# Performance work log

Measured on AMD Instinct MI355X. Metric: run time of the kernel, lower is better.

## Reference

```python
import jax, jax.numpy as jnp
import numpy as np

VECT = 300   # word-vector dim
H = 128      # GRU hidden size
NSTACK = 3   # MultiHead stacks (shared SelfAttention weights)
SEQ = 4096


def _ln(x, g, b, eps=1e-5):
    m = jnp.mean(x, axis=-1, keepdims=True)
    v = jnp.mean((x - m) ** 2, axis=-1, keepdims=True)
    return g * (x - m) / jnp.sqrt(v + eps) + b


def _multihead(x, q_w, q_b, k_w, k_b, v_w, v_b, aln_g, aln_b, w_w, w_b, mln_g, mln_b):
    # x: [S, 300]. Same attention weights reused for all 3 stacks (as in source).
    scale = jnp.sqrt(jnp.asarray(float(VECT), x.dtype))
    out = x
    for _ in range(NSTACK):
        q = out @ q_w.T + q_b
        k = out @ k_w.T + k_b
        v = out @ v_w.T + v_b
        a = jax.nn.softmax((q @ k.T) / scale, axis=1)      # [S, S]
        h = _ln(a @ v + out, aln_g, aln_b)                  # SelfAttention out
        out = _ln(h @ w_w.T + w_b + x, mln_g, mln_b)        # residual to original x
    return out


def _gru(xs, w_ih, w_hh, b_ih, b_hh):
    # xs: [S, VECT]; PyTorch GRUCell math, h0 = zeros. Input projections batched.
    gx = xs @ w_ih.T + b_ih  # [S, 3H]
    def step(h, g):
        gh = h @ w_hh.T + b_hh
        r = jax.nn.sigmoid(g[:H] + gh[:H])
        z = jax.nn.sigmoid(g[H:2 * H] + gh[H:2 * H])
        n = jnp.tanh(g[2 * H:] + r * gh[2 * H:])
        return (1.0 - z) * n + z * h, None
    h, _ = jax.lax.scan(step, jnp.zeros((H,), xs.dtype), gx)
    return h


def setup_inputs() -> dict:
    key = jax.random.key(0)
    ks = jax.random.split(key, 16)

    def lin(k, o, i, s=0.05):
        k1, k2 = jax.random.split(k)
        return (jax.random.normal(k1, (o, i), jnp.float32) * s,
                jax.random.normal(k2, (o,), jnp.float32) * s)

    q_w, q_b = lin(ks[0], VECT, VECT)
    k_w, k_b = lin(ks[1], VECT, VECT)
    v_w, v_b = lin(ks[2], VECT, VECT)
    w_w, w_b = lin(ks[3], VECT, VECT)
    g1_wih, g1_bih = lin(ks[4], 3 * H, VECT)
    g1_whh, g1_bhh = lin(ks[5], 3 * H, H)
    g2_wih, g2_bih = lin(ks[6], 3 * H, VECT)
    g2_whh, g2_bhh = lin(ks[7], 3 * H, H)
    fc1_w, fc1_b = lin(ks[8], 256, 2 * H)
    fc2_w, fc2_b = lin(ks[9], 3, 256)

    return {
        'x1': jax.random.normal(ks[10], (SEQ, VECT), jnp.float32),
        'x2': jax.random.normal(ks[11], (SEQ, VECT), jnp.float32),
        'q_w': q_w, 'q_b': q_b, 'k_w': k_w, 'k_b': k_b, 'v_w': v_w, 'v_b': v_b,
        'aln_g': jnp.ones((VECT,), jnp.float32), 'aln_b': jnp.zeros((VECT,), jnp.float32),
        'w_w': w_w, 'w_b': w_b,
        'mln_g': jnp.ones((VECT,), jnp.float32), 'mln_b': jnp.zeros((VECT,), jnp.float32),
        'g1_wih': g1_wih, 'g1_whh': g1_whh, 'g1_bih': g1_bih, 'g1_bhh': g1_bhh,
        'g2_wih': g2_wih, 'g2_whh': g2_whh, 'g2_bih': g2_bih, 'g2_bhh': g2_bhh,
        'fc1_w': fc1_w, 'fc1_b': fc1_b, 'fc2_w': fc2_w, 'fc2_b': fc2_b,
    }


def reference(x1, x2, q_w, q_b, k_w, k_b, v_w, v_b, aln_g, aln_b, w_w, w_b,
              mln_g, mln_b, g1_wih, g1_whh, g1_bih, g1_bhh,
              g2_wih, g2_whh, g2_bih, g2_bhh, fc1_w, fc1_b, fc2_w, fc2_b):
    a1 = _multihead(x1, q_w, q_b, k_w, k_b, v_w, v_b, aln_g, aln_b, w_w, w_b, mln_g, mln_b)
    a2 = _multihead(x2, q_w, q_b, k_w, k_b, v_w, v_b, aln_g, aln_b, w_w, w_b, mln_g, mln_b)
    h1 = _gru(a1, g1_wih, g1_whh, g1_bih, g1_bhh)  # [H]
    h2 = _gru(a2, g2_wih, g2_whh, g2_bih, g2_bhh)  # [H]
    h = jnp.concatenate([h1, h2])[None, :]          # [1, 2H]
    h = jax.nn.relu(h @ fc1_w.T + fc1_b)
    return jax.nn.log_softmax(h @ fc2_w.T + fc2_b, axis=1)  # [1, 3]
```

## Files before the change

### kernel.cpp

```cpp
#include <hip/hip_runtime.h>
#include <hip/hip_bf16.h>

#define SEQL 4096
#define VECT 300
#define DP   320
#define NQT  20
#define HN   128
#define G3   384
#define JC   4
#define KROW 328
#define VROW 40
#define PROW 40

typedef unsigned short u16;
typedef unsigned char  u8;
typedef __attribute__((ext_vector_type(8))) short bf16x8;
typedef __attribute__((ext_vector_type(4))) float f32x4;
typedef __attribute__((ext_vector_type(4))) unsigned int u32x4;
typedef __attribute__((ext_vector_type(8))) int   v8i;

#define MFMA(a,b,c) __builtin_amdgcn_mfma_f32_16x16x32_bf16(a,b,c,0,0,0)

#define L2E 1.44269504088896f

#define RAW_BAR() do {                                          \
    asm volatile("s_waitcnt lgkmcnt(0)" ::: "memory");          \
    __builtin_amdgcn_s_barrier();                               \
    asm volatile("" ::: "memory");                              \
} while (0)

__device__ __forceinline__ float bf2f(u16 v){
    union { unsigned u; float f; } t; t.u = ((unsigned)v) << 16; return t.f;
}
__device__ __forceinline__ u16 f2bf(float f){
    union { float f; unsigned u; } t; t.f = f;
    return (u16)((t.u + 0x7FFFu + ((t.u >> 16) & 1u)) >> 16);
}
__device__ __forceinline__ float sigm_f(float x){
    return __builtin_amdgcn_rcpf(1.f + __builtin_amdgcn_exp2f(-L2E * x));
}
__device__ __forceinline__ float tanh_f(float x){
    return fmaf(2.f, __builtin_amdgcn_rcpf(1.f + __builtin_amdgcn_exp2f(-2.f * L2E * x)), -1.f);
}
__device__ __forceinline__ float sel4(f32x4 v, int r){
    float a = (r & 1) ? v.y : v.x;
    float b = (r & 1) ? v.w : v.z;
    return (r & 2) ? b : a;
}

__global__ __launch_bounds__(256) void pad_x2(const float* __restrict__ x1, const float* __restrict__ x2,
                                              float* __restrict__ xf, u16* __restrict__ cur)
{
    int s = blockIdx.y;
    const float* src = s ? x2 : x1;
    float* xfo = xf + (long)s * SEQL * DP;
    u16*  cro = cur + (long)s * SEQL * DP;
    int n = SEQL * DP;
    for (int i = blockIdx.x * blockDim.x + threadIdx.x; i < n; i += gridDim.x * blockDim.x){
        int r = i / DP, c = i - r * DP;
        float v = (c < VECT) ? src[r * VECT + c] : 0.f;
        xfo[i] = v;
        cro[i] = f2bf(v);
    }
}

__global__ __launch_bounds__(256) void cvt_pad_w4(const float* __restrict__ w0, const float* __restrict__ w1,
                                                  const float* __restrict__ w2, const float* __restrict__ w3,
                                                  u16* __restrict__ Wpk)
{
    int sl = blockIdx.y;
    const float* src = (sl == 0) ? w0 : (sl == 1) ? w1 : (sl == 2) ? w2 : w3;
    u16* dst = Wpk + (long)sl * DP * DP;
    int n = DP * DP;
    for (int i = blockIdx.x * blockDim.x + threadIdx.x; i < n; i += gridDim.x * blockDim.x){
        int r = i / DP, c = i - r * DP;
        float v = (r < VECT && c < VECT) ? src[r * VECT + c] : 0.f;
        dst[i] = f2bf(v);
    }
}

__global__ __launch_bounds__(256) void cvt_pad_g2(const float* __restrict__ w0, const float* __restrict__ w1,
                                                  u16* __restrict__ GWpk)
{
    int s = blockIdx.y;
    const float* src = s ? w1 : w0;
    u16* dst = GWpk + (long)s * G3 * DP;
    int n = G3 * DP;
    for (int i = blockIdx.x * blockDim.x + threadIdx.x; i < n; i += gridDim.x * blockDim.x){
        int r = i / DP, c = i - r * DP;
        float v = (c < VECT) ? src[r * VECT + c] : 0.f;
        dst[i] = f2bf(v);
    }
}

__global__ __launch_bounds__(256) void cvt_whh2(const float* __restrict__ w0, const float* __restrict__ w1,
                                                u8* __restrict__ dst0)
{
    int s = blockIdx.y;
    const float* src = s ? w1 : w0;
    u8* dst = dst0 + (long)s * G3 * HN;
    int idx = blockIdx.x * 256 + threadIdx.x;
    if (idx >= G3 * HN) return;
    int prow = idx >> 7, col = idx & 127;
    int w  = prow / 48, rem = prow - w * 48;
    int g  = rem >> 4;  int rr = rem & 15;
    int orow = g * 128 + w * 16 + rr;
    int pk = __builtin_amdgcn_cvt_pk_fp8_f32(src[orow * HN + col], 0.f, 0, false);
    dst[idx] = (u8)(pk & 0xFF);
}

template<int NT, int OM, bool WPERSEQ>
__global__ __launch_bounds__(256) void gemm_k(
    const u16* __restrict__ A, const u16* __restrict__ Wp,
    const float* __restrict__ b0, const float* __restrict__ b1, const float* __restrict__ b2,
    int nb, void* __restrict__ Out)
{
    const int lane = threadIdx.x & 63;
    const int wid  = threadIdx.x >> 6;
    const int s    = blockIdx.z;
    const int sl   = blockIdx.y;
    const int wsel = WPERSEQ ? s : sl;
    const int row0 = blockIdx.x * 64 + wid * 16;
    const int m    = lane & 15;
    const int q    = lane >> 4;

    const u16* Arow = A + ((long)s * SEQL + row0) * DP;
    const u16* W    = Wp + (long)wsel * (NT * 16) * DP;

    f32x4 zf = {0.f, 0.f, 0.f, 0.f};
    f32x4 acc[NT];
    #pragma unroll
    for (int n = 0; n < NT; n++) acc[n] = zf;

    for (int c = 0; c < DP / 32; ++c){
        const int koff = c * 32 + q * 8;
        bf16x8 a0 = *(const bf16x8*)(Arow + m * DP + koff);
        #pragma unroll
        for (int n = 0; n < NT; n++){
            bf16x8 b = *(const bf16x8*)(W + (n * 16 + m) * DP + koff);
            acc[n] = MFMA(a0, b, acc[n]);
        }
    }

    const int bsel = WPERSEQ ? s : sl;
    const float* bp = (bsel == 0) ? b0 : ((bsel == 1) ? b1 : b2);
    const long SLC = 2L * SEQL * DP;

    #pragma unroll
    for (int n = 0; n < NT; n++){
        int col = n * 16 + m;
        float bv = (col < nb) ? bp[col] : 0.f;
        #pragma unroll
        for (int r = 0; r < 4; r++){
            long row = row0 + q * 4 + r;
            float v = acc[n][r] + bv;
            if (OM == 4){
                int g = col >> 7, i2 = col & 127;
                long off = ((long)s * SEQL + row) * (long)(NT * 16) + (i2 * 3 + g);
                ((float*)Out)[off] = v;
            } else {
                long off;
                if (sl < 2) off = ((long)(sl * 2 + s) * SEQL + row) * DP + col;
                else        off = 2 * SLC + ((long)s * DP + col) * SEQL + row;
                ((u16*)Out)[off] = f2bf(v);
            }
        }
    }
}

__global__ __launch_bounds__(256) void gemmln_k(
    const u16* __restrict__ A, const u16* __restrict__ Wp, const float* __restrict__ bias,
    const float* __restrict__ res0, const float* __restrict__ res1,
    const float* __restrict__ g, const float* __restrict__ b,
    u16* __restrict__ OutB, float* __restrict__ OutF)
{
    const int lane = threadIdx.x & 63;
    const int wid  = threadIdx.x >> 6;
    const int s    = blockIdx.z;
    const int row0 = blockIdx.x * 64 + wid * 16;
    const int m    = lane & 15;
    const int q    = lane >> 4;

    const u16* Arow = A + ((long)s * SEQL + row0) * DP;
    const float* res = s ? res1 : res0;

    f32x4 zf = {0.f, 0.f, 0.f, 0.f};
    f32x4 acc[NQT];
    #pragma unroll
    for (int n = 0; n < NQT; n++) acc[n] = zf;

    for (int c = 0; c < DP / 32; ++c){
        const int koff = c * 32 + q * 8;
        bf16x8 a0 = *(const bf16x8*)(Arow + m * DP + koff);
        #pragma unroll
        for (int n = 0; n < NQT; n++){
            bf16x8 bb = *(const bf16x8*)(Wp + (n * 16 + m) * DP + koff);
            acc[n] = MFMA(a0, bb, acc[n]);
        }
    }

    float sum[4] = {0,0,0,0}, sq[4] = {0,0,0,0};
    #pragma unroll
    for (int n = 0; n < NQT; n++){
        int col = n * 16 + m;
        float bv = (col < VECT) ? bias[col] : 0.f;
        #pragma unroll
        for (int r = 0; r < 4; r++){
            long row = row0 + q * 4 + r;
            float rr = (col < VECT) ? res[row * VECT + col] : 0.f;
            float t = (col < VECT) ? (acc[n][r] + bv + rr) : 0.f;
            acc[n][r] = t;
            sum[r] += t; sq[r] += t * t;
        }
    }
    #pragma unroll
    for (int r = 0; r < 4; r++){
        float su = sum[r], sv = sq[r];
        su += __shfl_xor(su, 1); sv += __shfl_xor(sv, 1);
        su += __shfl_xor(su, 2); sv += __shfl_xor(sv, 2);
        su += __shfl_xor(su, 4); sv += __shfl_xor(sv, 4);
        su += __shfl_xor(su, 8); sv += __shfl_xor(sv, 8);
        sum[r] = su; sq[r] = sv;
    }
    float mean[4], rstd[4];
    #pragma unroll
    for (int r = 0; r < 4; r++){
        mean[r] = sum[r] / VECT;
        float var = sq[r] / VECT - mean[r] * mean[r];
        rstd[r] = rsqrtf(var + 1e-5f);
    }
    #pragma unroll
    for (int n = 0; n < NQT; n++){
        int col = n * 16 + m;
        float gv = (col < VECT) ? g[col] : 0.f;
        float bv = (col < VECT) ? b[col] : 0.f;
        #pragma unroll
        for (int r = 0; r < 4; r++){
            long row = (long)s * SEQL + row0 + q * 4 + r;
            float t = (col < VECT) ? ((acc[n][r] - mean[r]) * rstd[r] * gv + bv) : 0.f;
            OutB[row * DP + col] = f2bf(t);
            OutF[row * DP + col] = t;
        }
    }
}

__global__ __launch_bounds__(256, 2) void flash_k(
    const u16* __restrict__ Q, const u16* __restrict__ K, const u16* __restrict__ VT,
    u16* __restrict__ Onum, float* __restrict__ Lp)
{
    const int tid  = threadIdx.x;
    const int lane = tid & 63;
    const int wid  = tid >> 6;
    const int bid  = blockIdx.x;
    const int s    = bid & 1;
    const int jc   = (bid >> 1) & 3;
    const int xi   = bid >> 3;
    const int row0 = xi * 64 + wid * 16;
    const int m = lane & 15, q = lane >> 4;

    __shared__ __align__(16) u16 Kt[32 * KROW];
    __shared__ __align__(16) u16 Vt[DP * VROW];
    __shared__ __align__(16) u16 pb[4][16 * PROW];

    const u16* Qb = Q  + ((long)s * SEQL + row0) * DP;
    const u16* Kc = K  + (long)s * SEQL * DP + (long)jc * 1024 * DP;
    const u16* Vc = VT + (long)s * DP * SEQL + jc * 1024;

    bf16x8 qf[10];
    #pragma unroll
    for (int c = 0; c < 10; c++)
        qf[c] = *(const bf16x8*)(Qb + m * DP + c * 32 + q * 8);

    int skoff[5], wkoff[5], svoff[5], wvoff[5];
    #pragma unroll
    for (int it = 0; it < 5; it++){
        int f  = (it * 256 + tid) * 8;
        int rk = f / 320, ck = f - rk * 320;
        skoff[it] = f;
        wkoff[it] = rk * KROW + ck;
        int rv = f >> 5, cv = f & 31;
        svoff[it] = rv * SEQL + cv;
        wvoff[it] = rv * VROW + cv;
    }

    f32x4 zf = {0.f, 0.f, 0.f, 0.f};
    f32x4 oacc[NQT];
    #pragma unroll
    for (int n = 0; n < NQT; n++) oacc[n] = zf;
    float lacc[4] = {0,0,0,0};

    const float K2 = 0.057735026918962576f * L2E;
    const float MB = -16.f * L2E;

    u32x4 kreg[5], vreg[5];
    #pragma unroll
    for (int it = 0; it < 5; it++){
        kreg[it] = *(const u32x4*)(Kc + skoff[it]);
        vreg[it] = *(const u32x4*)(Vc + svoff[it]);
    }
    #pragma unroll
    for (int it = 0; it < 5; it++){
        *(u32x4*)(&Kt[wkoff[it]]) = kreg[it];
        *(u32x4*)(&Vt[wvoff[it]]) = vreg[it];
    }
    RAW_BAR();

    u16* pbw = &pb[wid][0];

    for (int j = 0; j < 32; ++j){
        if (j + 1 < 32){
            const u16* Kj = Kc + (j + 1) * 32 * DP;
            const u16* Vj = Vc + (j + 1) * 32;
            #pragma unroll
            for (int it = 0; it < 5; it++){
                kreg[it] = *(const u32x4*)(Kj + skoff[it]);
                vreg[it] = *(const u32x4*)(Vj + svoff[it]);
            }
        }
        f32x4 sA = zf, sB = zf;
        #pragma unroll
        for (int c = 0; c < 10; c++){
            bf16x8 kA = *(const bf16x8*)(&Kt[(m     ) * KROW + c * 32 + q * 8]);
            bf16x8 kB = *(const bf16x8*)(&Kt[(m + 16) * KROW + c * 32 + q * 8]);
            sA = MFMA(qf[c], kA, sA);
            sB = MFMA(qf[c], kB, sB);
        }
        #pragma unroll
        for (int r = 0; r < 4; r++){
            float a = __builtin_amdgcn_exp2f(fmaf(sA[r], K2, MB));
            float b = __builtin_amdgcn_exp2f(fmaf(sB[r], K2, MB));
            lacc[r] += a + b;
            pbw[(q * 4 + r) * PROW +      m] = f2bf(a);
            pbw[(q * 4 + r) * PROW + 16 + m] = f2bf(b);
        }
        bf16x8 pf = *(const bf16x8*)(&pbw[m * PROW + q * 8]);
        #pragma unroll
        for (int n = 0; n < NQT; n++){
            bf16x8 vb = *(const bf16x8*)(&Vt[(n * 16 + m) * VROW + q * 8]);
            oacc[n] = MFMA(pf, vb, oacc[n]);
        }
        RAW_BAR();
        if (j + 1 < 32){
            #pragma unroll
            for (int it = 0; it < 5; it++){
                *(u32x4*)(&Kt[wkoff[it]]) = kreg[it];
                *(u32x4*)(&Vt[wvoff[it]]) = vreg[it];
            }
        }
        RAW_BAR();
    }

    #pragma unroll
    for (int r = 0; r < 4; r++){
        float t0 = lacc[r];
        t0 += __shfl_xor(t0, 1); t0 += __shfl_xor(t0, 2);
        t0 += __shfl_xor(t0, 4); t0 += __shfl_xor(t0, 8);
        lacc[r] = t0;
    }
    const long grow0 = (long)s * SEQL + row0;
    if (m == 0){
        #pragma unroll
        for (int r = 0; r < 4; r++)
            Lp[(long)jc * 2 * SEQL + grow0 + q * 4 + r] = lacc[r];
    }
    u16* Ob = Onum + ((long)jc * 2 * SEQL + grow0) * DP;
    #pragma unroll
    for (int n = 0; n < NQT; n++)
        #pragma unroll
        for (int r = 0; r < 4; r++)
            Ob[(long)(q * 4 + r) * DP + n * 16 + m] = f2bf(oacc[n][r]);
}

__global__ __launch_bounds__(256) void lncomb_k(const u16* __restrict__ Onum, const float* __restrict__ Lp,
                                                const float* __restrict__ XF,
                                                const float* __restrict__ g, const float* __restrict__ b,
                                                u16* __restrict__ OutB)
{
    long row = (long)((blockIdx.x * blockDim.x + threadIdx.x) >> 6);
    int lane = threadIdx.x & 63;
    if (row >= 2L * SEQL) return;
    float l = 0.f;
    #pragma unroll
    for (int jc = 0; jc < JC; jc++) l += Lp[(long)jc * 2 * SEQL + row];
    float inv = 1.f / l;
    const float* xr = XF + row * DP;
    float v[5], sum = 0.f, sq = 0.f;
    #pragma unroll
    for (int i = 0; i < 5; i++){
        int c = lane + i * 64;
        float o = 0.f;
        #pragma unroll
        for (int jc = 0; jc < JC; jc++)
            o += bf2f(Onum[((long)jc * 2 * SEQL + row) * DP + c]);
        float t = (c < VECT) ? (o * inv + xr[c]) : 0.f;
        v[i] = t; sum += t; sq += t * t;
    }
    #pragma unroll
    for (int o = 1; o < 64; o <<= 1){ sum += __shfl_xor(sum, o); sq += __shfl_xor(sq, o); }
    float mean = sum / VECT;
    float var  = sq / VECT - mean * mean;
    float rstd = rsqrtf(var + 1e-5f);
    #pragma unroll
    for (int i = 0; i < 5; i++){
        int c = lane + i * 64;
        float t = (c < VECT) ? ((v[i] - mean) * rstd * g[c] + b[c]) : 0.f;
        OutB[row * DP + c] = f2bf(t);
    }
}

__global__ __launch_bounds__(512, 1) void gru_k(
    const float* __restrict__ GXP,
    const u8* __restrict__ Whh8p,
    const float* __restrict__ Bhh1, const float* __restrict__ Bhh2,
    float* __restrict__ Hout)
{
    const int s = blockIdx.x;
    const int tid = threadIdx.x;
    const int lane = tid & 63;
    const int wid  = tid >> 6;
    const int m = lane & 15, q = lane >> 4;
    const u8* Whh = Whh8p + (long)s * G3 * HN;
    const float* Bhh = s ? Bhh2 : Bhh1;
    const float* gx = GXP + (long)s * SEQL * G3;

    __shared__ __align__(8) u8 hst[2][HN];

    v8i af[3];
    #pragma unroll
    for (int g = 0; g < 3; g++)
        af[g] = *(const v8i*)(Whh + (long)(wid * 48 + g * 16 + m) * HN + q * 32);

    const int rsel = m & 3;
    const int il   = wid * 16 + q * 4 + rsel;
    const int il3  = il * 3;
    const float bhr = Bhh[il], bhz = Bhh[HN + il], bhn = Bhh[2 * HN + il];

    if (tid < HN){ hst[0][tid] = 0; hst[1][tid] = 0; }

    const float* ga = gx + il3;
    float cr0 = ga[0], cz0 = ga[1], cn0 = ga[2];
    const float* gb = gx + G3 + il3;
    float cr1 = gb[0], cz1 = gb[1], cn1 = gb[2];

    __syncthreads();

    float h = 0.f;
    const f32x4 zf = {0.f, 0.f, 0.f, 0.f};

#define GRU_STEP(T, CR, CZ, CN, WB, RB)                                               \
    {                                                                                 \
        v8i bfrag = *(const v8i*)(&hst[RB][q * 32]);                                  \
        f32x4 a0 = __builtin_amdgcn_mfma_scale_f32_16x16x128_f8f6f4(af[0], bfrag, zf, 0, 0, 0, 127, 0, 127); \
        f32x4 a1 = __builtin_amdgcn_mfma_scale_f32_16x16x128_f8f6f4(af[1], bfrag, zf, 0, 0, 0, 127, 0, 127); \
        f32x4 a2 = __builtin_amdgcn_mfma_scale_f32_16x16x128_f8f6f4(af[2], bfrag, zf, 0, 0, 0, 127, 0, 127); \
        float ghr = sel4(a0, rsel);                                                   \
        float ghz = sel4(a1, rsel);                                                   \
        float ghn = sel4(a2, rsel);                                                   \
        float rg = sigm_f(CR + ghr + bhr);                                            \
        float zg = sigm_f(CZ + ghz + bhz);                                            \
        float ng = tanh_f(CN + rg * (ghn + bhn));                                     \
        h = (1.f - zg) * ng + zg * h;                                                 \
        if (m < 4){                                                                   \
            int pk = __builtin_amdgcn_cvt_pk_fp8_f32(h, h, 0, false);                 \
            hst[WB][il] = (u8)(pk & 0xFF);                                            \
        }                                                                             \
        int tp = ((T) + 2 < SEQL) ? (T) + 2 : SEQL - 1;                               \
        const float* gp = gx + (long)tp * G3 + il3;                                   \
        CR = gp[0]; CZ = gp[1]; CN = gp[2];                                           \
        asm volatile("s_waitcnt lgkmcnt(0)" ::: "memory");                            \
        __builtin_amdgcn_s_barrier();                                                 \
        asm volatile("" ::: "memory");                                                \
    }

    for (int t = 0; t < SEQL; t += 2){
        GRU_STEP(t,     cr0, cz0, cn0, 0, 1);
        GRU_STEP(t + 1, cr1, cz1, cn1, 1, 0);
    }
#undef GRU_STEP

    if (m < 4) Hout[s * HN + il] = h;
}

__global__ __launch_bounds__(256) void final_k(const float* __restrict__ Hout,
                                               const float* __restrict__ fc1w, const float* __restrict__ fc1b,
                                               const float* __restrict__ fc2w, const float* __restrict__ fc2b,
                                               float* __restrict__ out)
{
    __shared__ float hb[256];
    __shared__ float r1[256];
    __shared__ float lg[3];
    int tid = threadIdx.x;
    hb[tid] = Hout[tid];
    __syncthreads();
    float a = 0.f;
    for (int k2 = 0; k2 < 256; k2++) a += hb[k2] * fc1w[tid * 256 + k2];
    a += fc1b[tid];
    r1[tid] = fmaxf(a, 0.f);
    __syncthreads();
    if (tid < 3){
        float v = 0.f;
        for (int k2 = 0; k2 < 256; k2++) v += r1[k2] * fc2w[tid * 256 + k2];
        lg[tid] = v + fc2b[tid];
    }
    __syncthreads();
    if (tid == 0){
        float mx = fmaxf(lg[0], fmaxf(lg[1], lg[2]));
        float se = __expf(lg[0] - mx) + __expf(lg[1] - mx) + __expf(lg[2] - mx);
        float ls = mx + logf(se);
        out[0] = lg[0] - ls;
        out[1] = lg[1] - ls;
        out[2] = lg[2] - ls;
    }
}

extern "C" void kernel_launch(void* const* d_in, const int* in_sizes, int n_in,
                              void* d_out, int out_size, void* d_ws, size_t ws_size,
                              hipStream_t stream)
{
    (void)in_sizes; (void)n_in; (void)out_size; (void)ws_size;
    const float* x1     = (const float*)d_in[0];
    const float* x2     = (const float*)d_in[1];
    const float* q_w    = (const float*)d_in[2],  *q_b   = (const float*)d_in[3];
    const float* k_w    = (const float*)d_in[4],  *k_b   = (const float*)d_in[5];
    const float* v_w    = (const float*)d_in[6],  *v_b   = (const float*)d_in[7];
    const float* aln_g  = (const float*)d_in[8],  *aln_b = (const float*)d_in[9];
    const float* w_w    = (const float*)d_in[10], *w_b   = (const float*)d_in[11];
    const float* mln_g  = (const float*)d_in[12], *mln_b = (const float*)d_in[13];
    const float* g1_wih = (const float*)d_in[14], *g1_whh = (const float*)d_in[15];
    const float* g1_bih = (const float*)d_in[16], *g1_bhh = (const float*)d_in[17];
    const float* g2_wih = (const float*)d_in[18], *g2_whh = (const float*)d_in[19];
    const float* g2_bih = (const float*)d_in[20], *g2_bhh = (const float*)d_in[21];
    const float* fc1w   = (const float*)d_in[22], *fc1b  = (const float*)d_in[23];
    const float* fc2w   = (const float*)d_in[24], *fc2b  = (const float*)d_in[25];

    char* wsp = (char*)d_ws;
    auto alloc = [&](size_t bytes) -> char* {
        char* p = wsp; wsp += (bytes + 255) & ~(size_t)255; return p;
    };
    float* XF   = (float*)alloc(2L * SEQL * DP * 4);
    u16*   CUR  = (u16*)  alloc(2L * SEQL * DP * 2);
    u16*   Hb   = (u16*)  alloc(2L * SEQL * DP * 2);
    u16*   Wpk  = (u16*)  alloc(4L * DP * DP * 2);
    u16*   GWpk = (u16*)  alloc(2L * G3 * DP * 2);
    u8*    Whh8 = (u8*)   alloc(2L * G3 * HN);
    float* Hout = (float*)alloc(2L * HN * 4);
    float* Lp   = (float*)alloc((long)JC * 2 * SEQL * 4);
    size_t u1 = (2L * 2 * SEQL * DP + 2L * DP * SEQL) * 2;
    size_t u1b = 2L * SEQL * G3 * 4;
    u16*   QKV  = (u16*)  alloc(u1 > u1b ? u1 : u1b);
    u16*   VT   = QKV + 2L * 2 * SEQL * DP;
    float* GX   = (float*)QKV;
    u16*   Onum = (u16*)  alloc((long)JC * 2 * SEQL * DP * 2);

    pad_x2<<<dim3(256, 2), 256, 0, stream>>>(x1, x2, XF, CUR);
    cvt_pad_w4<<<dim3(128, 4), 256, 0, stream>>>(q_w, k_w, v_w, w_w, Wpk);
    cvt_pad_g2<<<dim3(128, 2), 256, 0, stream>>>(g1_wih, g2_wih, GWpk);
    cvt_whh2<<<dim3(192, 2), 256, 0, stream>>>(g1_whh, g2_whh, Whh8);

    for (int st = 0; st < 3; ++st){
        gemm_k<NQT, 3, false><<<dim3(SEQL / 64, 3, 2), 256, 0, stream>>>(
            CUR, Wpk, q_b, k_b, v_b, VECT, QKV);
        flash_k<<<dim3(512), 256, 0, stream>>>(QKV, QKV + 2L*SEQL*DP, VT, Onum, Lp);
        lncomb_k<<<dim3(2 * SEQL / 4), 256, 0, stream>>>(Onum, Lp, XF, aln_g, aln_b, Hb);
        gemmln_k<<<dim3(SEQL / 64, 1, 2), 256, 0, stream>>>(
            Hb, Wpk + 3L * DP * DP, w_b, x1, x2, mln_g, mln_b, CUR, XF);
    }

    gemm_k<24, 4, true><<<dim3(SEQL / 64, 1, 2), 256, 0, stream>>>(
        CUR, GWpk, g1_bih, g2_bih, nullptr, G3, GX);
    gru_k<<<dim3(2), 512, 0, stream>>>(GX, Whh8, g1_bhh, g2_bhh, Hout);
    final_k<<<dim3(1), 256, 0, stream>>>(Hout, fc1w, fc1b, fc2w, fc2b, (float*)d_out);
}
```

Measured before the change: 2.008 ms.

## Fuse attention LayerNorm combine into output-projection GEMM via folded weights

Removes the separate lncomb kernel and the Hb intermediate buffer. The split-KV partial sums are combined per row inside the GEMM kernel, staged in LDS as bf16, and the first LayerNorm is applied after the matmul algebraically. The LN gamma is folded into the weight matrix, and the mean correction and beta contribution come from precomputed row sums. This saves one launch and a global write and read of the normalized activations per stack, at the cost of GEMM on un-normalized bf16 values (precision risk) and a small extra prep kernel.

After: 2.036 ms. No clear change (+1.4%).

```diff
diff --git a/kernel.cpp b/kernel.cpp
--- a/kernel.cpp
+++ b/kernel.cpp
@@ -11,6 +11,7 @@
 #define KROW 328
 #define VROW 40
 #define PROW 40
+#define AROW 328
 
 typedef unsigned short u16;
 typedef unsigned char  u8;
@@ -64,18 +65,44 @@
     }
 }
 
-__global__ __launch_bounds__(256) void cvt_pad_w4(const float* __restrict__ w0, const float* __restrict__ w1,
-                                                  const float* __restrict__ w2, const float* __restrict__ w3,
+__global__ __launch_bounds__(256) void cvt_pad_w3(const float* __restrict__ w0, const float* __restrict__ w1,
+                                                  const float* __restrict__ w2,
                                                   u16* __restrict__ Wpk)
 {
     int sl = blockIdx.y;
-    const float* src = (sl == 0) ? w0 : (sl == 1) ? w1 : (sl == 2) ? w2 : w3;
+    const float* src = (sl == 0) ? w0 : (sl == 1) ? w1 : w2;
     u16* dst = Wpk + (long)sl * DP * DP;
     int n = DP * DP;
     for (int i = blockIdx.x * blockDim.x + threadIdx.x; i < n; i += gridDim.x * blockDim.x){
         int r = i / DP, c = i - r * DP;
         float v = (r < VECT && c < VECT) ? src[r * VECT + c] : 0.f;
         dst[i] = f2bf(v);
+    }
+}
+
+__global__ __launch_bounds__(320) void prep_wln(const float* __restrict__ w_w,
+                                                const float* __restrict__ ag, const float* __restrict__ ab,
+                                                u16* __restrict__ WLN,
+                                                float* __restrict__ gWsum, float* __restrict__ bW)
+{
+    int out = blockIdx.x;
+    int c   = threadIdx.x;
+    float wv = (out < VECT && c < VECT) ? w_w[out * VECT + c] : 0.f;
+    float gv = (c < VECT) ? ag[c] : 0.f;
+    float bv = (c < VECT) ? ab[c] : 0.f;
+    float wp = gv * wv;
+    WLN[(long)out * DP + c] = f2bf(wp);
+    float s1 = wp, s2 = bv * wv;
+    #pragma unroll
+    for (int o = 1; o < 64; o <<= 1){ s1 += __shfl_xor(s1, o); s2 += __shfl_xor(s2, o); }
+    __shared__ float r1[5], r2[5];
+    if ((c & 63) == 0){ r1[c >> 6] = s1; r2[c >> 6] = s2; }
+    __syncthreads();
+    if (c == 0){
+        float a = 0.f, b2 = 0.f;
+        #pragma unroll
+        for (int i = 0; i < 5; i++){ a += r1[i]; b2 += r2[i]; }
+        gWsum[out] = a; bW[out] = b2;
     }
 }
 
@@ -168,10 +195,12 @@
     }
 }
 
-__global__ __launch_bounds__(256) void gemmln_k(
-    const u16* __restrict__ A, const u16* __restrict__ Wp, const float* __restrict__ bias,
+__global__ __launch_bounds__(256) void fuse2_k(
+    const u16* __restrict__ Onum, const float* __restrict__ Lp, const float* __restrict__ XF,
+    const u16* __restrict__ WLN, const float* __restrict__ gWsum, const float* __restrict__ bW,
+    const float* __restrict__ wb,
     const float* __restrict__ res0, const float* __restrict__ res1,
-    const float* __restrict__ g, const float* __restrict__ b,
+    const float* __restrict__ mg, const float* __restrict__ mb,
     u16* __restrict__ OutB, float* __restrict__ OutF)
 {
     const int lane = threadIdx.x & 63;
@@ -181,8 +210,40 @@
     const int m    = lane & 15;
     const int q    = lane >> 4;
 
-    const u16* Arow = A + ((long)s * SEQL + row0) * DP;
-    const float* res = s ? res1 : res0;
+    __shared__ __align__(16) u16 At[4][16 * AROW];
+
+    const long grow = (long)s * SEQL + row0 + m;
+    float l = 0.f;
+    #pragma unroll
+    for (int jc = 0; jc < JC; jc++) l += Lp[(long)jc * 2 * SEQL + grow];
+    float inv = 1.f / l;
+    const float* xr = XF + grow * DP;
+    float sum = 0.f, sq = 0.f;
+    #pragma unroll
+    for (int i = 0; i < 10; i++){
+        int c0 = q * 80 + i * 8;
+        float o[8] = {0,0,0,0,0,0,0,0};
+        #pragma unroll
+        for (int jc = 0; jc < JC; jc++){
+            bf16x8 ov = *(const bf16x8*)(Onum + ((long)jc * 2 * SEQL + grow) * DP + c0);
+            #pragma unroll
+            for (int e = 0; e < 8; e++) o[e] += bf2f(((u16*)&ov)[e]);
+        }
+        u16 st[8];
+        #pragma unroll
+        for (int e = 0; e < 8; e++){
+            int c = c0 + e;
+            float t = (c < VECT) ? (o[e] * inv + xr[c]) : 0.f;
+            sum += t; sq += t * t;
+            st[e] = f2bf(t);
+        }
+        *(bf16x8*)(&At[wid][m * AROW + c0]) = *(bf16x8*)st;
+    }
+    sum += __shfl_xor(sum, 16); sq += __shfl_xor(sq, 16);
+    sum += __shfl_xor(sum, 32); sq += __shfl_xor(sq, 32);
+    float mean = sum / VECT;
+    float var  = sq / VECT - mean * mean;
+    float rstd = rsqrtf(var + 1e-5f);
 
     f32x4 zf = {0.f, 0.f, 0.f, 0.f};
     f32x4 acc[NQT];
@@ -191,53 +252,64 @@
 
     for (int c = 0; c < DP / 32; ++c){
         const int koff = c * 32 + q * 8;
-        bf16x8 a0 = *(const bf16x8*)(Arow + m * DP + koff);
+        bf16x8 a0 = *(const bf16x8*)(&At[wid][m * AROW + koff]);
         #pragma unroll
         for (int n = 0; n < NQT; n++){
-            bf16x8 bb = *(const bf16x8*)(Wp + (n * 16 + m) * DP + koff);
+            bf16x8 bb = *(const bf16x8*)(WLN + (long)(n * 16 + m) * DP + koff);
             acc[n] = MFMA(a0, bb, acc[n]);
         }
     }
 
-    float sum[4] = {0,0,0,0}, sq[4] = {0,0,0,0};
+    float mean_r[4], rstd_r[4];
+    #pragma unroll
+    for (int r = 0; r < 4; r++){
+        mean_r[r] = __shfl(mean, q * 4 + r);
+        rstd_r[r] = __shfl(rstd, q * 4 + r);
+    }
+
+    const float* res = s ? res1 : res0;
+    float sum2[4] = {0,0,0,0}, sq2[4] = {0,0,0,0};
     #pragma unroll
     for (int n = 0; n < NQT; n++){
         int col = n * 16 + m;
-        float bv = (col < VECT) ? bias[col] : 0.f;
+        float gws = gWsum[col];
+        float bWv = bW[col];
+        float wbv = (col < VECT) ? wb[col] : 0.f;
         #pragma unroll
         for (int r = 0; r < 4; r++){
             long row = row0 + q * 4 + r;
             float rr = (col < VECT) ? res[row * VECT + col] : 0.f;
-            float t = (col < VECT) ? (acc[n][r] + bv + rr) : 0.f;
+            float y = rstd_r[r] * (acc[n][r] - mean_r[r] * gws) + bWv + wbv + rr;
+            float t = (col < VECT) ? y : 0.f;
             acc[n][r] = t;
-            sum[r] += t; sq[r] += t * t;
+            sum2[r] += t; sq2[r] += t * t;
         }
     }
     #pragma unroll
     for (int r = 0; r < 4; r++){
-        float su = sum[r], sv = sq[r];
+        float su = sum2[r], sv = sq2[r];
         su += __shfl_xor(su, 1); sv += __shfl_xor(sv, 1);
         su += __shfl_xor(su, 2); sv += __shfl_xor(sv, 2);
         su += __shfl_xor(su, 4); sv += __shfl_xor(sv, 4);
         su += __shfl_xor(su, 8); sv += __shfl_xor(sv, 8);
-        sum[r] = su; sq[r] = sv;
-    }
-    float mean[4], rstd[4];
+        sum2[r] = su; sq2[r] = sv;
+    }
+    float mean2[4], rstd2[4];
     #pragma unroll
     for (int r = 0; r < 4; r++){
-        mean[r] = sum[r] / VECT;
-        float var = sq[r] / VECT - mean[r] * mean[r];
-        rstd[r] = rsqrtf(var + 1e-5f);
+        mean2[r] = sum2[r] / VECT;
+        float v2 = sq2[r] / VECT - mean2[r] * mean2[r];
+        rstd2[r] = rsqrtf(v2 + 1e-5f);
     }
     #pragma unroll
     for (int n = 0; n < NQT; n++){
         int col = n * 16 + m;
-        float gv = (col < VECT) ? g[col] : 0.f;
-        float bv = (col < VECT) ? b[col] : 0.f;
+        float gv = (col < VECT) ? mg[col] : 0.f;
+        float bv = (col < VECT) ? mb[col] : 0.f;
         #pragma unroll
         for (int r = 0; r < 4; r++){
             long row = (long)s * SEQL + row0 + q * 4 + r;
-            float t = (col < VECT) ? ((acc[n][r] - mean[r]) * rstd[r] * gv + bv) : 0.f;
+            float t = (col < VECT) ? ((acc[n][r] - mean2[r]) * rstd2[r] * gv + bv) : 0.f;
             OutB[row * DP + col] = f2bf(t);
             OutF[row * DP + col] = t;
         }
@@ -369,43 +441,6 @@
         #pragma unroll
         for (int r = 0; r < 4; r++)
             Ob[(long)(q * 4 + r) * DP + n * 16 + m] = f2bf(oacc[n][r]);
-}
-
-__global__ __launch_bounds__(256) void lncomb_k(const u16* __restrict__ Onum, const float* __restrict__ Lp,
-                                                const float* __restrict__ XF,
-                                                const float* __restrict__ g, const float* __restrict__ b,
-                                                u16* __restrict__ OutB)
-{
-    long row = (long)((blockIdx.x * blockDim.x + threadIdx.x) >> 6);
-    int lane = threadIdx.x & 63;
-    if (row >= 2L * SEQL) return;
-    float l = 0.f;
-    #pragma unroll
-    for (int jc = 0; jc < JC; jc++) l += Lp[(long)jc * 2 * SEQL + row];
-    float inv = 1.f / l;
-    const float* xr = XF + row * DP;
-    float v[5], sum = 0.f, sq = 0.f;
-    #pragma unroll
-    for (int i = 0; i < 5; i++){
-        int c = lane + i * 64;
-        float o = 0.f;
-        #pragma unroll
-        for (int jc = 0; jc < JC; jc++)
-            o += bf2f(Onum[((long)jc * 2 * SEQL + row) * DP + c]);
-        float t = (c < VECT) ? (o * inv + xr[c]) : 0.f;
-        v[i] = t; sum += t; sq += t * t;
-    }
-    #pragma unroll
-    for (int o = 1; o < 64; o <<= 1){ sum += __shfl_xor(sum, o); sq += __shfl_xor(sq, o); }
-    float mean = sum / VECT;
-    float var  = sq / VECT - mean * mean;
-    float rstd = rsqrtf(var + 1e-5f);
-    #pragma unroll
-    for (int i = 0; i < 5; i++){
-        int c = lane + i * 64;
-        float t = (c < VECT) ? ((v[i] - mean) * rstd * g[c] + b[c]) : 0.f;
-        OutB[row * DP + c] = f2bf(t);
-    }
 }
 
 __global__ __launch_bounds__(512, 1) void gru_k(
@@ -539,8 +574,10 @@
     };
     float* XF   = (float*)alloc(2L * SEQL * DP * 4);
     u16*   CUR  = (u16*)  alloc(2L * SEQL * DP * 2);
-    u16*   Hb   = (u16*)  alloc(2L * SEQL * DP * 2);
-    u16*   Wpk  = (u16*)  alloc(4L * DP * DP * 2);
+    u16*   Wpk  = (u16*)  alloc(3L * DP * DP * 2);
+    u16*   WLN  = (u16*)  alloc(1L * DP * DP * 2);
+    float* gWsum= (float*)alloc(DP * 4);
+    float* bW   = (float*)alloc(DP * 4);
     u16*   GWpk = (u16*)  alloc(2L * G3 * DP * 2);
     u8*    Whh8 = (u8*)   alloc(2L * G3 * HN);
     float* Hout = (float*)alloc(2L * HN * 4);
@@ -553,7 +590,8 @@
     u16*   Onum = (u16*)  alloc((long)JC * 2 * SEQL * DP * 2);
 
     pad_x2<<<dim3(256, 2), 256, 0, stream>>>(x1, x2, XF, CUR);
-    cvt_pad_w4<<<dim3(128, 4), 256, 0, stream>>>(q_w, k_w, v_w, w_w, Wpk);
+    cvt_pad_w3<<<dim3(128, 3), 256, 0, stream>>>(q_w, k_w, v_w, Wpk);
+    prep_wln<<<dim3(DP), 320, 0, stream>>>(w_w, aln_g, aln_b, WLN, gWsum, bW);
     cvt_pad_g2<<<dim3(128, 2), 256, 0, stream>>>(g1_wih, g2_wih, GWpk);
     cvt_whh2<<<dim3(192, 2), 256, 0, stream>>>(g1_whh, g2_whh, Whh8);
 
@@ -561,9 +599,8 @@
         gemm_k<NQT, 3, false><<<dim3(SEQL / 64, 3, 2), 256, 0, stream>>>(
             CUR, Wpk, q_b, k_b, v_b, VECT, QKV);
         flash_k<<<dim3(512), 256, 0, stream>>>(QKV, QKV + 2L*SEQL*DP, VT, Onum, Lp);
-        lncomb_k<<<dim3(2 * SEQL / 4), 256, 0, stream>>>(Onum, Lp, XF, aln_g, aln_b, Hb);
-        gemmln_k<<<dim3(SEQL / 64, 1, 2), 256, 0, stream>>>(
-            Hb, Wpk + 3L * DP * DP, w_b, x1, x2, mln_g, mln_b, CUR, XF);
+        fuse2_k<<<dim3(SEQL / 64, 1, 2), 256, 0, stream>>>(
+            Onum, Lp, XF, WLN, gWsum, bW, w_b, x1, x2, mln_g, mln_b, CUR, XF);
     }
 
     gemm_k<24, 4, true><<<dim3(SEQL / 64, 1, 2), 256, 0, stream>>>(
```
